# Kernel optimization log

Hardware: AMD Instinct MI355X
Metric: run time of the kernel (lower is better)

The kernel has to match this reference:

```python
import jax, jax.numpy as jnp
import numpy as np

NEG_SLOPE = 0.2
EPS = 1e-16

N_NODES = 100000
N_EDGES = 1600000
F_IN = 64
HID = 64
T_OUT = 1


def _gat_conv(x, src, dst, W, a_src, a_dst, b, n_nodes):
    # x: [N, Fin] -> h: [N, H]
    h = x @ W
    # per-node attention logits, then gather per-edge (PyG GATConv, heads=1)
    s_src = h @ a_src  # [N]
    s_dst = h @ a_dst  # [N]
    e = jax.nn.leaky_relu(s_src[src] + s_dst[dst], NEG_SLOPE)  # [E]
    # segment softmax over incoming edges of each destination node
    m = jax.ops.segment_max(e, dst, num_segments=n_nodes)  # [N]
    ex = jnp.exp(e - m[dst])
    denom = jax.ops.segment_sum(ex, dst, num_segments=n_nodes)  # [N]
    alpha = ex / (denom[dst] + EPS)  # [E]
    # weighted scatter-add aggregation
    out = jax.ops.segment_sum(alpha[:, None] * h[src], dst, num_segments=n_nodes)
    return out + b


def _add_self_loops(edge_index, n_nodes):
    loops = jnp.arange(n_nodes, dtype=edge_index.dtype)
    src = jnp.concatenate([edge_index[0], loops])
    dst = jnp.concatenate([edge_index[1], loops])
    return src, dst


def setup_inputs() -> dict:
    key = jax.random.key(0)
    ks = jax.random.split(key, 12)
    x = jax.random.normal(ks[0], (N_NODES, F_IN), dtype=jnp.float32)
    edge_index = jax.random.randint(ks[1], (2, N_EDGES), 0, N_NODES, dtype=jnp.int32)
    s1 = 1.0 / np.sqrt(F_IN)
    s2 = 1.0 / np.sqrt(HID)
    return {
        "x": x,
        "edge_index": edge_index,
        "W1": jax.random.normal(ks[2], (F_IN, HID), dtype=jnp.float32) * s1,
        "a_src1": jax.random.normal(ks[3], (HID,), dtype=jnp.float32) * s2,
        "a_dst1": jax.random.normal(ks[4], (HID,), dtype=jnp.float32) * s2,
        "b1": jnp.zeros((HID,), dtype=jnp.float32),
        "W2": jax.random.normal(ks[5], (HID, HID), dtype=jnp.float32) * s2,
        "a_src2": jax.random.normal(ks[6], (HID,), dtype=jnp.float32) * s2,
        "a_dst2": jax.random.normal(ks[7], (HID,), dtype=jnp.float32) * s2,
        "b2": jnp.zeros((HID,), dtype=jnp.float32),
        "Wl": jax.random.normal(ks[8], (HID, T_OUT), dtype=jnp.float32) * s2,
        "bl": jnp.zeros((T_OUT,), dtype=jnp.float32),
    }


def reference(x, edge_index, W1, a_src1, a_dst1, b1, W2, a_src2, a_dst2, b2, Wl, bl):
    n_nodes = x.shape[0]
    src, dst = _add_self_loops(edge_index, n_nodes)  # PyG add_self_loops=True
    h = _gat_conv(x, src, dst, W1, a_src1, a_dst1, b1, n_nodes)
    h = jnp.tanh(h)  # dropout is identity in eval mode
    h = _gat_conv(h, src, dst, W2, a_src2, a_dst2, b2, n_nodes)
    return h @ Wl + bl  # [N, 1]
```

## Files before the change

### kernel.cpp

```cpp
#include <hip/hip_runtime.h>

#define NN 100000
#define NE 1600000
#define ET (NE + NN)
#define NB 391
#define CAP 5120
#define BST 16
#define NBIN 256
#define NCHK (ET/8)
#define NTILE (NN/16)

typedef _Float16 f16;
typedef __attribute__((ext_vector_type(8))) _Float16 half8;
typedef __attribute__((ext_vector_type(4))) float f32x4;

__device__ __forceinline__ unsigned short hbits(float v){
    f16 h = (f16)v;
    return *(unsigned short*)&h;
}
__device__ __forceinline__ unsigned pk16(float a, float b){
    auto p = __builtin_amdgcn_cvt_pkrtz(a, b);
    return *(unsigned*)&p;
}
__device__ __forceinline__ float fast_tanh(float x){
    float e = __expf(2.f*x);
    return 1.f - __fdividef(2.f, e + 1.f);
}
__device__ __forceinline__ void fmix2(float& al, float& ah, unsigned h2, float a){
    asm("v_fma_mix_f32 %0, %2, %3, %0 op_sel_hi:[1,0,0]\n\t"
        "v_fma_mix_f32 %1, %2, %3, %1 op_sel:[1,0,0] op_sel_hi:[1,0,0]"
        : "+v"(al), "+v"(ah) : "v"(h2), "v"(a));
}

__global__ void __launch_bounds__(256) k_bin(const int* __restrict__ src,
        const int* __restrict__ dst, int* __restrict__ bcnt,
        int* __restrict__ binbuf){
    __shared__ int cnt[NB];
    __shared__ int cur[NB];
    int t = threadIdx.x;
    for(int i=t;i<NB;i+=256) cnt[i]=0;
    __syncthreads();
    for(int g = blockIdx.x*256 + t; g < NCHK; g += NBIN*256){
        if(g < NE/8){
            const uint4* dp = (const uint4*)(dst + g*8);
            uint4 d0 = dp[0], d1 = dp[1];
            atomicAdd(&cnt[d0.x>>8],1); atomicAdd(&cnt[d0.y>>8],1);
            atomicAdd(&cnt[d0.z>>8],1); atomicAdd(&cnt[d0.w>>8],1);
            atomicAdd(&cnt[d1.x>>8],1); atomicAdd(&cnt[d1.y>>8],1);
            atomicAdd(&cnt[d1.z>>8],1); atomicAdd(&cnt[d1.w>>8],1);
        } else {
            int n0 = g*8 - NE;
            #pragma unroll
            for(int i=0;i<8;i++) atomicAdd(&cnt[(n0+i)>>8],1);
        }
    }
    __syncthreads();
    for(int i=t;i<NB;i+=256){ int c=cnt[i]; cur[i] = c ? atomicAdd(&bcnt[i*BST], c) : 0; }
    __syncthreads();
    for(int g = blockIdx.x*256 + t; g < NCHK; g += NBIN*256){
        int s[8], d[8];
        if(g < NE/8){
            const uint4* sp = (const uint4*)(src + g*8);
            const uint4* dp = (const uint4*)(dst + g*8);
            uint4 s0 = sp[0], s1 = sp[1];
            uint4 d0 = dp[0], d1 = dp[1];
            s[0]=s0.x; s[1]=s0.y; s[2]=s0.z; s[3]=s0.w;
            s[4]=s1.x; s[5]=s1.y; s[6]=s1.z; s[7]=s1.w;
            d[0]=d0.x; d[1]=d0.y; d[2]=d0.z; d[3]=d0.w;
            d[4]=d1.x; d[5]=d1.y; d[6]=d1.z; d[7]=d1.w;
        } else {
            int n0 = g*8 - NE;
            #pragma unroll
            for(int i=0;i<8;i++){ s[i]=n0+i; d[i]=n0+i; }
        }
        #pragma unroll
        for(int i=0;i<8;i++){
            int b = d[i] >> 8;
            int pos = atomicAdd(&cur[b], 1);
            if(pos < CAP) binbuf[b*CAP + pos] = (s[i] << 8) | (d[i] & 255);
        }
    }
}

__global__ void __launch_bounds__(256) k_build(const int* __restrict__ bcnt,
        const int* __restrict__ binbuf, int* __restrict__ edge_src,
        int2* __restrict__ rd){
    __shared__ int lsrc[CAP];
    __shared__ int ldeg[256], lscan[256], lcur[256], red[256];
    int b = blockIdx.x, t = threadIdx.x;
    int cnt = min(bcnt[b*BST], CAP);
    int part = 0;
    for(int i=t;i<b;i+=256) part += min(bcnt[i*BST], CAP);
    red[t] = part; __syncthreads();
    for(int off=128; off>=1; off>>=1){ if(t<off) red[t]+=red[t+off]; __syncthreads(); }
    int base = red[0];
    __syncthreads();
    ldeg[t] = 0; __syncthreads();
    const int* bb = binbuf + b*CAP;
    for(int i=t;i<cnt;i+=256) atomicAdd(&ldeg[bb[i] & 255], 1);
    __syncthreads();
    int dv = ldeg[t]; lscan[t] = dv; __syncthreads();
    for(int off=1; off<256; off<<=1){
        int u = (t>=off) ? lscan[t-off] : 0;
        __syncthreads(); lscan[t] += u; __syncthreads();
    }
    int excl = lscan[t] - dv; lcur[t] = excl;
    int node = b*256 + t;
    if(node < NN) rd[node] = make_int2(base + excl, dv);
    __syncthreads();
    for(int i=t;i<cnt;i+=256){
        int ent = bb[i];
        int pos = atomicAdd(&lcur[ent & 255], 1);
        lsrc[pos] = ent >> 8;
    }
    __syncthreads();
    for(int i=t;i<cnt;i+=256) edge_src[base+i] = lsrc[i];
}

template<int FPIN, int L2>
__global__ void __launch_bounds__(256) k_gemm(const void* __restrict__ xin,
        const float* __restrict__ W, const float* __restrict__ avs,
        const float* __restrict__ avd, const float* __restrict__ Wlv,
        f16* __restrict__ hb, float* __restrict__ ssrc,
        float* __restrict__ sdst, float* __restrict__ gsc){
    int tid = threadIdx.x, lane = tid & 63;
    int col = lane & 15, q = lane >> 4;
    half8 Bf[2][4];
    #pragma unroll
    for(int kh=0;kh<2;kh++){
        #pragma unroll
        for(int nb=0;nb<4;nb++){
            half8 b;
            #pragma unroll
            for(int j=0;j<8;j++){
                float w = W[(kh*32 + q*8 + j)*64 + nb*16 + col];
                b[j] = (f16)w;
            }
            Bf[kh][nb] = b;
        }
    }
    float as[4], ad[4], wl[4];
    #pragma unroll
    for(int nb=0;nb<4;nb++){
        as[nb] = avs[nb*16+col]; ad[nb] = avd[nb*16+col];
        wl[nb] = L2 ? Wlv[nb*16+col] : 0.f;
    }

    int gw = (blockIdx.x*256 + tid) >> 6;
    int nwaves = gridDim.x*4;
    for(int tile = gw; tile < NTILE; tile += nwaves){
        int n0 = tile*16;
        f32x4 acc[4];
        #pragma unroll
        for(int nb=0;nb<4;nb++) acc[nb] = (f32x4){0.f,0.f,0.f,0.f};
        #pragma unroll
        for(int kh=0;kh<2;kh++){
            half8 a;
            if(FPIN){
                const float4* xr = (const float4*)((const float*)xin
                                    + (size_t)(n0+col)*64 + kh*32 + q*8);
                float4 u = xr[0], v = xr[1];
                union { half8 h; uint4 u4; } A;
                A.u4.x = pk16(u.x, u.y);
                A.u4.y = pk16(u.z, u.w);
                A.u4.z = pk16(v.x, v.y);
                A.u4.w = pk16(v.z, v.w);
                a = A.h;
            } else {
                a = *(const half8*)((const f16*)xin
                                    + (size_t)(n0+col)*64 + kh*32 + q*8);
            }
            #pragma unroll
            for(int nb=0;nb<4;nb++)
                acc[nb] = __builtin_amdgcn_mfma_f32_16x16x32_f16(a, Bf[kh][nb], acc[nb], 0,0,0);
        }
        if(!L2){
            #pragma unroll
            for(int nb=0;nb<4;nb++){
                #pragma unroll
                for(int r=0;r<4;r++)
                    hb[(size_t)(n0 + q*4 + r)*64 + nb*16 + col] = (f16)acc[nb][r];
            }
        }
        #pragma unroll
        for(int r=0;r<4;r++){
            float ps = acc[0][r]*as[0] + acc[1][r]*as[1] + acc[2][r]*as[2] + acc[3][r]*as[3];
            float pd = acc[0][r]*ad[0] + acc[1][r]*ad[1] + acc[2][r]*ad[2] + acc[3][r]*ad[3];
            float pg = L2 ? (acc[0][r]*wl[0] + acc[1][r]*wl[1] + acc[2][r]*wl[2] + acc[3][r]*wl[3]) : 0.f;
            #pragma unroll
            for(int m=8;m>=1;m>>=1){
                ps += __shfl_xor(ps,m); pd += __shfl_xor(pd,m);
                if(L2) pg += __shfl_xor(pg,m);
            }
            if(col == 0){
                ssrc[n0 + q*4 + r] = ps; sdst[n0 + q*4 + r] = pd;
                if(L2) gsc[n0 + q*4 + r] = pg;
            }
        }
    }
}

__device__ __forceinline__ void node_full1(int node, int lane, int2* lp,
        const int2* __restrict__ rd, const int* __restrict__ edge_src,
        const float* __restrict__ ssrc, const float* __restrict__ sdst,
        const f16* __restrict__ hb, const float* __restrict__ bias,
        f16* __restrict__ out1b){
    int2 r = rd[node];
    int rs = r.x, d = r.y;
    float sd = sdst[node];
    int g8 = lane >> 3;
    int c  = lane & 7;
    float a0=0.f,a1=0.f,a2=0.f,a3=0.f,a4=0.f,a5=0.f,a6=0.f,a7=0.f;

    float lmax = -1e30f;
    for(int j=lane; j<d; j+=64){
        int sj = edge_src[rs+j];
        float t = ssrc[sj] + sd;
        lmax = fmaxf(lmax, fmaxf(t, 0.2f*t));
    }
    #pragma unroll
    for(int m=32;m>=1;m>>=1) lmax = fmaxf(lmax, __shfl_xor(lmax,m));
    float lsum = 0.f;
    for(int j=lane; j<d; j+=64){
        int sj = edge_src[rs+j];
        float t = ssrc[sj] + sd;
        lsum += __expf(fmaxf(t, 0.2f*t) - lmax);
    }
    #pragma unroll
    for(int m=32;m>=1;m>>=1) lsum += __shfl_xor(lsum,m);
    float inv = 1.0f/(lsum + 1e-16f);
    for(int cb=0; cb<d; cb+=64){
        int s2 = 0; float al = 0.f;
        int j = cb + lane;
        if(j < d){
            s2 = edge_src[rs+j];
            float t = ssrc[s2] + sd;
            al = __expf(fmaxf(t, 0.2f*t) - lmax) * inv;
        }
        lp[lane] = make_int2(__float_as_int(al), s2);
        int dd = min(d - cb, 64);
        for(int i0=0; i0<dd; i0+=16){
            int2 e0 = lp[i0 + g8];
            int2 e1 = lp[i0 + 8 + g8];
            float f0 = __int_as_float(e0.x);
            float f1 = __int_as_float(e1.x);
            uint4 k0 = *(const uint4*)(hb + ((size_t)e0.y<<6) + (c<<3));
            uint4 k1 = *(const uint4*)(hb + ((size_t)e1.y<<6) + (c<<3));
            fmix2(a0,a1,k0.x,f0); fmix2(a2,a3,k0.y,f0);
            fmix2(a4,a5,k0.z,f0); fmix2(a6,a7,k0.w,f0);
            fmix2(a0,a1,k1.x,f1); fmix2(a2,a3,k1.y,f1);
            fmix2(a4,a5,k1.z,f1); fmix2(a6,a7,k1.w,f1);
        }
    }
    #pragma unroll
    for(int m=32;m>=8;m>>=1){
        a0 += __shfl_xor(a0,m); a1 += __shfl_xor(a1,m);
        a2 += __shfl_xor(a2,m); a3 += __shfl_xor(a3,m);
        a4 += __shfl_xor(a4,m); a5 += __shfl_xor(a5,m);
        a6 += __shfl_xor(a6,m); a7 += __shfl_xor(a7,m);
    }
    const float4* bp = (const float4*)bias;
    float4 bv0 = bp[c*2], bv1 = bp[c*2+1];
    if(g8 == 0){
        uint4 o;
        o.x = (unsigned)hbits(fast_tanh(a0+bv0.x)) | ((unsigned)hbits(fast_tanh(a1+bv0.y))<<16);
        o.y = (unsigned)hbits(fast_tanh(a2+bv0.z)) | ((unsigned)hbits(fast_tanh(a3+bv0.w))<<16);
        o.z = (unsigned)hbits(fast_tanh(a4+bv1.x)) | ((unsigned)hbits(fast_tanh(a5+bv1.y))<<16);
        o.w = (unsigned)hbits(fast_tanh(a6+bv1.z)) | ((unsigned)hbits(fast_tanh(a7+bv1.w))<<16);
        *(uint4*)(out1b + ((size_t)node<<6) + (c<<3)) = o;
    }
}

__global__ void __launch_bounds__(256) k_agg1(
        const int2* __restrict__ rd, const int* __restrict__ edge_src,
        const float* __restrict__ ssrc, const float* __restrict__ sdst,
        const f16* __restrict__ hb, const float* __restrict__ bias,
        f16* __restrict__ out1b){
    __shared__ int2 pairs[256];
    int tid = threadIdx.x;
    int wv   = (blockIdx.x*256 + tid) >> 6;
    int lane = tid & 63;
    if(wv*2 >= NN) return;
    int2* lp = pairs + (tid & 192);
    int half = lane >> 5, l = lane & 31;
    int node = wv*2 + half;

    int2 r = rd[node];
    int rs = r.x, d = r.y;
    float sd = sdst[node];
    int dmax = max(d, __shfl_xor(d, 32));

    if(dmax <= 32){
        int s = 0; float pr = 0.f;
        if(l < d){
            s = edge_src[rs + l];
            float t = ssrc[s] + sd;
            t = fmaxf(t, 0.2f*t);
            pr = __expf(fminf(t, 80.f));
        }
        float sm = pr;
        #pragma unroll
        for(int m=16;m>=1;m>>=1) sm += __shfl_xor(sm,m);
        float alpha = pr * (1.0f/(sm + 1e-16f));
        lp[lane] = make_int2(__float_as_int(alpha), s);

        int g4 = l >> 3;
        int c  = l & 7;
        int base = half << 5;
        int nitw = (dmax + 7) >> 3;
        float F0[4], F1[4];
        uint4 K0[4], K1[4];
        #pragma unroll
        for(int it=0; it<4; it++){
            if(it < nitw){
                int2 e0 = lp[base + it*8 + g4];
                int2 e1 = lp[base + it*8 + 4 + g4];
                F0[it] = __int_as_float(e0.x);
                F1[it] = __int_as_float(e1.x);
                K0[it] = *(const uint4*)(hb + ((size_t)e0.y<<6) + (c<<3));
                K1[it] = *(const uint4*)(hb + ((size_t)e1.y<<6) + (c<<3));
            }
        }
        float a0=0.f,a1=0.f,a2=0.f,a3=0.f,a4=0.f,a5=0.f,a6=0.f,a7=0.f;
        #pragma unroll
        for(int it=0; it<4; it++){
            if(it < nitw){
                fmix2(a0,a1,K0[it].x,F0[it]); fmix2(a2,a3,K0[it].y,F0[it]);
                fmix2(a4,a5,K0[it].z,F0[it]); fmix2(a6,a7,K0[it].w,F0[it]);
                fmix2(a0,a1,K1[it].x,F1[it]); fmix2(a2,a3,K1[it].y,F1[it]);
                fmix2(a4,a5,K1[it].z,F1[it]); fmix2(a6,a7,K1[it].w,F1[it]);
            }
        }

        bool b3 = (l >> 3) & 1, b4 = (l >> 4) & 1;
        float u0 = b3 ? a4 : a0, v0 = b3 ? a0 : a4; u0 += __shfl_xor(v0, 8);
        float u1 = b3 ? a5 : a1, v1 = b3 ? a1 : a5; u1 += __shfl_xor(v1, 8);
        float u2 = b3 ? a6 : a2, v2 = b3 ? a2 : a6; u2 += __shfl_xor(v2, 8);
        float u3 = b3 ? a7 : a3, v3 = b3 ? a3 : a7; u3 += __shfl_xor(v3, 8);
        float w0 = b4 ? u2 : u0, z0 = b4 ? u0 : u2; w0 += __shfl_xor(z0, 16);
        float w1 = b4 ? u3 : u1, z1 = b4 ? u1 : u3; w1 += __shfl_xor(z1, 16);
        int ch0 = (c<<3) + ((int)b3<<2) + ((int)b4<<1);

        float2 bv = ((const float2*)bias)[ch0>>1];
        unsigned o = pk16(fast_tanh(w0 + bv.x), fast_tanh(w1 + bv.y));
        *(unsigned*)(out1b + ((size_t)node<<6) + ch0) = o;
    } else {
        node_full1(wv*2,   lane, lp, rd, edge_src, ssrc, sdst, hb, bias, out1b);
        node_full1(wv*2+1, lane, lp, rd, edge_src, ssrc, sdst, hb, bias, out1b);
    }
}

__global__ void __launch_bounds__(256) k_agg2(
        const int2* __restrict__ rd, const int* __restrict__ edge_src,
        const float* __restrict__ ssrc, const float* __restrict__ sdst,
        const float* __restrict__ gsc, const float* __restrict__ bias,
        const float* __restrict__ Wl, const float* __restrict__ bl,
        float* __restrict__ outF){
    int tid = threadIdx.x;
    int wv   = (blockIdx.x*256 + tid) >> 6;
    int lane = tid & 63;
    if(wv*2 >= NN) return;
    int half = lane >> 5, l = lane & 31;
    int node = wv*2 + half;

    float2 bv = ((const float2*)bias)[l];
    float2 wl = ((const float2*)Wl)[l];
    float rc = bv.x*wl.x + bv.y*wl.y;
    #pragma unroll
    for(int m=16;m>=1;m>>=1) rc += __shfl_xor(rc,m);

    int2 r = rd[node];
    int rs = r.x, d = r.y;
    float sd = sdst[node];
    int dmax = max(d, __shfl_xor(d, 32));

    if(dmax <= 32){
        float pr = 0.f, gv = 0.f;
        if(l < d){
            int s = edge_src[rs + l];
            float t = ssrc[s] + sd;
            t = fmaxf(t, 0.2f*t);
            pr = __expf(fminf(t, 80.f));
            gv = gsc[s];
        }
        float sm = pr, num = pr*gv;
        #pragma unroll
        for(int m=16;m>=1;m>>=1){ sm += __shfl_xor(sm,m); num += __shfl_xor(num,m); }
        if(l == 0) outF[node] = num/(sm + 1e-16f) + rc + bl[0];
    } else {
        #pragma unroll 1
        for(int k=0;k<2;k++){
            int nd = wv*2 + k;
            int2 r2 = rd[nd];
            int rs2 = r2.x, d2 = r2.y;
            float sd2 = sdst[nd];
            float lmax = -1e30f;
            for(int j=lane; j<d2; j+=64){
                int sj = edge_src[rs2+j];
                float t = ssrc[sj] + sd2;
                lmax = fmaxf(lmax, fmaxf(t, 0.2f*t));
            }
            #pragma unroll
            for(int m=32;m>=1;m>>=1) lmax = fmaxf(lmax, __shfl_xor(lmax,m));
            float lsum = 0.f, lnum = 0.f;
            for(int j=lane; j<d2; j+=64){
                int sj = edge_src[rs2+j];
                float t = ssrc[sj] + sd2;
                float e = __expf(fmaxf(t, 0.2f*t) - lmax);
                lsum += e; lnum += e*gsc[sj];
            }
            #pragma unroll
            for(int m=32;m>=1;m>>=1){ lsum += __shfl_xor(lsum,m); lnum += __shfl_xor(lnum,m); }
            if(lane == 0) outF[nd] = lnum/(lsum + 1e-16f) + rc + bl[0];
        }
    }
}

extern "C" void kernel_launch(void* const* d_in, const int* in_sizes, int n_in,
                              void* d_out, int out_size, void* d_ws, size_t ws_size,
                              hipStream_t stream) {
    const float* x   = (const float*)d_in[0];
    const int*   ei  = (const int*)d_in[1];
    const float* W1  = (const float*)d_in[2];
    const float* as1 = (const float*)d_in[3];
    const float* ad1 = (const float*)d_in[4];
    const float* b1  = (const float*)d_in[5];
    const float* W2  = (const float*)d_in[6];
    const float* as2 = (const float*)d_in[7];
    const float* ad2 = (const float*)d_in[8];
    const float* b2  = (const float*)d_in[9];
    const float* Wl  = (const float*)d_in[10];
    const float* bl  = (const float*)d_in[11];
    float* out = (float*)d_out;

    const int* srcp = ei;
    const int* dstp = ei + NE;

    char* w = (char*)d_ws;
    int*   edge_src = (int*)w;  w += (size_t)ET*4;
    f16*   hb       = (f16*)w;  w += (size_t)NN*64*2;
    f16*   t1b      = (f16*)w;  w += (size_t)NN*64*2;
    int2*  rd       = (int2*)w; w += (size_t)NN*8;
    float* ssrc     = (float*)w; w += (size_t)NN*4;
    float* sdst     = (float*)w; w += (size_t)NN*4;
    float* gsc      = (float*)w; w += (size_t)NN*4;
    int*   bcnt     = (int*)w;  w += (size_t)NB*BST*4;
    int*   binbuf   = (int*)hb;

    const int nbG  = 782;
    const int nbA1 = (NN/2 + 3)/4;
    const int nbA2 = (NN/2 + 3)/4;

    (void)hipMemsetAsync(bcnt, 0, (size_t)NB*BST*4, stream);
    k_bin  <<<NBIN, 256, 0, stream>>>(srcp, dstp, bcnt, binbuf);
    k_build<<<NB,   256, 0, stream>>>(bcnt, binbuf, edge_src, rd);

    k_gemm<1,0><<<nbG, 256, 0, stream>>>((const void*)x, W1, as1, ad1,
                                         (const float*)nullptr, hb, ssrc, sdst,
                                         (float*)nullptr);
    k_agg1<<<nbA1, 256, 0, stream>>>(rd, edge_src, ssrc, sdst, hb, b1, t1b);
    k_gemm<0,1><<<nbG, 256, 0, stream>>>((const void*)t1b, W2, as2, ad2, Wl,
                                         (f16*)nullptr, ssrc, sdst, gsc);
    k_agg2<<<nbA2, 256, 0, stream>>>(rd, edge_src, ssrc, sdst, gsc,
                                     b2, Wl, bl, out);
}
```

Baseline: 196.6 us.

## Fold layer-2 GEMM into per-node vectors and fuse CSR build with layer-1 GEMM

Layer 2 only needs the attention scores and the final linear projection of h2, so W2·a_src2, W2·a_dst2 and W2·Wl are precomputed into three 64-vectors. The layer-1 aggregation then emits the three scalar scores per node directly. This drops the tanh output buffer, the second GEMM kernel and its 100k×64 f16 round trip. The CSR build and the layer-1 GEMM are merged into one launch split by block index so they can overlap, and binbuf gets its own buffer instead of aliasing hb. The cost is extra shuffle reductions in agg1 and reassociating the sums, which changes rounding slightly.

```diff
diff --git a/kernel.cpp b/kernel.cpp
--- a/kernel.cpp
+++ b/kernel.cpp
@@ -9,6 +9,7 @@
 #define NBIN 256
 #define NCHK (ET/8)
 #define NTILE (NN/16)
+#define NBG 782
 
 typedef _Float16 f16;
 typedef __attribute__((ext_vector_type(8))) _Float16 half8;
@@ -30,6 +31,19 @@
     asm("v_fma_mix_f32 %0, %2, %3, %0 op_sel_hi:[1,0,0]\n\t"
         "v_fma_mix_f32 %1, %2, %3, %1 op_sel:[1,0,0] op_sel_hi:[1,0,0]"
         : "+v"(al), "+v"(ah) : "v"(h2), "v"(a));
+}
+
+__global__ void __launch_bounds__(64) k_pre(const float* __restrict__ W2,
+        const float* __restrict__ as2, const float* __restrict__ ad2,
+        const float* __restrict__ Wl, float* __restrict__ w2v){
+    int j = threadIdx.x;
+    float s = 0.f, d = 0.f, g = 0.f;
+    #pragma unroll 8
+    for(int i=0;i<64;i++){
+        float w = W2[j*64 + i];
+        s += w*as2[i]; d += w*ad2[i]; g += w*Wl[i];
+    }
+    w2v[j] = s; w2v[64+j] = d; w2v[128+j] = g;
 }
 
 __global__ void __launch_bounds__(256) k_bin(const int* __restrict__ src,
@@ -82,82 +96,76 @@
     }
 }
 
-__global__ void __launch_bounds__(256) k_build(const int* __restrict__ bcnt,
-        const int* __restrict__ binbuf, int* __restrict__ edge_src,
-        int2* __restrict__ rd){
+__global__ void __launch_bounds__(256) k_bg(
+        const int* __restrict__ bcnt, const int* __restrict__ binbuf,
+        int* __restrict__ edge_src, int2* __restrict__ rd,
+        const float* __restrict__ xin, const float* __restrict__ W,
+        const float* __restrict__ avs, const float* __restrict__ avd,
+        f16* __restrict__ hb, float* __restrict__ ssrc,
+        float* __restrict__ sdst){
     __shared__ int lsrc[CAP];
     __shared__ int ldeg[256], lscan[256], lcur[256], red[256];
-    int b = blockIdx.x, t = threadIdx.x;
-    int cnt = min(bcnt[b*BST], CAP);
-    int part = 0;
-    for(int i=t;i<b;i+=256) part += min(bcnt[i*BST], CAP);
-    red[t] = part; __syncthreads();
-    for(int off=128; off>=1; off>>=1){ if(t<off) red[t]+=red[t+off]; __syncthreads(); }
-    int base = red[0];
-    __syncthreads();
-    ldeg[t] = 0; __syncthreads();
-    const int* bb = binbuf + b*CAP;
-    for(int i=t;i<cnt;i+=256) atomicAdd(&ldeg[bb[i] & 255], 1);
-    __syncthreads();
-    int dv = ldeg[t]; lscan[t] = dv; __syncthreads();
-    for(int off=1; off<256; off<<=1){
-        int u = (t>=off) ? lscan[t-off] : 0;
-        __syncthreads(); lscan[t] += u; __syncthreads();
-    }
-    int excl = lscan[t] - dv; lcur[t] = excl;
-    int node = b*256 + t;
-    if(node < NN) rd[node] = make_int2(base + excl, dv);
-    __syncthreads();
-    for(int i=t;i<cnt;i+=256){
-        int ent = bb[i];
-        int pos = atomicAdd(&lcur[ent & 255], 1);
-        lsrc[pos] = ent >> 8;
-    }
-    __syncthreads();
-    for(int i=t;i<cnt;i+=256) edge_src[base+i] = lsrc[i];
-}
-
-template<int FPIN, int L2>
-__global__ void __launch_bounds__(256) k_gemm(const void* __restrict__ xin,
-        const float* __restrict__ W, const float* __restrict__ avs,
-        const float* __restrict__ avd, const float* __restrict__ Wlv,
-        f16* __restrict__ hb, float* __restrict__ ssrc,
-        float* __restrict__ sdst, float* __restrict__ gsc){
-    int tid = threadIdx.x, lane = tid & 63;
-    int col = lane & 15, q = lane >> 4;
-    half8 Bf[2][4];
-    #pragma unroll
-    for(int kh=0;kh<2;kh++){
-        #pragma unroll
-        for(int nb=0;nb<4;nb++){
-            half8 b;
-            #pragma unroll
-            for(int j=0;j<8;j++){
-                float w = W[(kh*32 + q*8 + j)*64 + nb*16 + col];
-                b[j] = (f16)w;
-            }
-            Bf[kh][nb] = b;
-        }
-    }
-    float as[4], ad[4], wl[4];
-    #pragma unroll
-    for(int nb=0;nb<4;nb++){
-        as[nb] = avs[nb*16+col]; ad[nb] = avd[nb*16+col];
-        wl[nb] = L2 ? Wlv[nb*16+col] : 0.f;
-    }
-
-    int gw = (blockIdx.x*256 + tid) >> 6;
-    int nwaves = gridDim.x*4;
-    for(int tile = gw; tile < NTILE; tile += nwaves){
-        int n0 = tile*16;
-        f32x4 acc[4];
-        #pragma unroll
-        for(int nb=0;nb<4;nb++) acc[nb] = (f32x4){0.f,0.f,0.f,0.f};
+    int t = threadIdx.x;
+    if(blockIdx.x < NB){
+        int b = blockIdx.x;
+        int cnt = min(bcnt[b*BST], CAP);
+        int part = 0;
+        for(int i=t;i<b;i+=256) part += min(bcnt[i*BST], CAP);
+        red[t] = part; __syncthreads();
+        for(int off=128; off>=1; off>>=1){ if(t<off) red[t]+=red[t+off]; __syncthreads(); }
+        int base = red[0];
+        __syncthreads();
+        ldeg[t] = 0; __syncthreads();
+        const int* bb = binbuf + b*CAP;
+        for(int i=t;i<cnt;i+=256) atomicAdd(&ldeg[bb[i] & 255], 1);
+        __syncthreads();
+        int dv = ldeg[t]; lscan[t] = dv; __syncthreads();
+        for(int off=1; off<256; off<<=1){
+            int u = (t>=off) ? lscan[t-off] : 0;
+            __syncthreads(); lscan[t] += u; __syncthreads();
+        }
+        int excl = lscan[t] - dv; lcur[t] = excl;
+        int node = b*256 + t;
+        if(node < NN) rd[node] = make_int2(base + excl, dv);
+        __syncthreads();
+        for(int i=t;i<cnt;i+=256){
+            int ent = bb[i];
+            int pos = atomicAdd(&lcur[ent & 255], 1);
+            lsrc[pos] = ent >> 8;
+        }
+        __syncthreads();
+        for(int i=t;i<cnt;i+=256) edge_src[base+i] = lsrc[i];
+    } else {
+        int lane = t & 63;
+        int col = lane & 15, q = lane >> 4;
+        half8 Bf[2][4];
         #pragma unroll
         for(int kh=0;kh<2;kh++){
-            half8 a;
-            if(FPIN){
-                const float4* xr = (const float4*)((const float*)xin
+            #pragma unroll
+            for(int nb=0;nb<4;nb++){
+                half8 bfr;
+                #pragma unroll
+                for(int j=0;j<8;j++){
+                    float w = W[(kh*32 + q*8 + j)*64 + nb*16 + col];
+                    bfr[j] = (f16)w;
+                }
+                Bf[kh][nb] = bfr;
+            }
+        }
+        float as[4], ad[4];
+        #pragma unroll
+        for(int nb=0;nb<4;nb++){ as[nb] = avs[nb*16+col]; ad[nb] = avd[nb*16+col]; }
+
+        int gw = ((blockIdx.x - NB)*256 + t) >> 6;
+        int nwaves = NBG*4;
+        for(int tile = gw; tile < NTILE; tile += nwaves){
+            int n0 = tile*16;
+            f32x4 acc[4];
+            #pragma unroll
+            for(int nb=0;nb<4;nb++) acc[nb] = (f32x4){0.f,0.f,0.f,0.f};
+            #pragma unroll
+            for(int kh=0;kh<2;kh++){
+                const float4* xr = (const float4*)(xin
                                     + (size_t)(n0+col)*64 + kh*32 + q*8);
                 float4 u = xr[0], v = xr[1];
                 union { half8 h; uint4 u4; } A;
@@ -165,36 +173,23 @@
                 A.u4.y = pk16(u.z, u.w);
                 A.u4.z = pk16(v.x, v.y);
                 A.u4.w = pk16(v.z, v.w);
-                a = A.h;
-            } else {
-                a = *(const half8*)((const f16*)xin
-                                    + (size_t)(n0+col)*64 + kh*32 + q*8);
-            }
-            #pragma unroll
-            for(int nb=0;nb<4;nb++)
-                acc[nb] = __builtin_amdgcn_mfma_f32_16x16x32_f16(a, Bf[kh][nb], acc[nb], 0,0,0);
-        }
-        if(!L2){
+                #pragma unroll
+                for(int nb=0;nb<4;nb++)
+                    acc[nb] = __builtin_amdgcn_mfma_f32_16x16x32_f16(A.h, Bf[kh][nb], acc[nb], 0,0,0);
+            }
             #pragma unroll
             for(int nb=0;nb<4;nb++){
                 #pragma unroll
                 for(int r=0;r<4;r++)
                     hb[(size_t)(n0 + q*4 + r)*64 + nb*16 + col] = (f16)acc[nb][r];
             }
-        }
-        #pragma unroll
-        for(int r=0;r<4;r++){
-            float ps = acc[0][r]*as[0] + acc[1][r]*as[1] + acc[2][r]*as[2] + acc[3][r]*as[3];
-            float pd = acc[0][r]*ad[0] + acc[1][r]*ad[1] + acc[2][r]*ad[2] + acc[3][r]*ad[3];
-            float pg = L2 ? (acc[0][r]*wl[0] + acc[1][r]*wl[1] + acc[2][r]*wl[2] + acc[3][r]*wl[3]) : 0.f;
-            #pragma unroll
-            for(int m=8;m>=1;m>>=1){
-                ps += __shfl_xor(ps,m); pd += __shfl_xor(pd,m);
-                if(L2) pg += __shfl_xor(pg,m);
-            }
-            if(col == 0){
-                ssrc[n0 + q*4 + r] = ps; sdst[n0 + q*4 + r] = pd;
-                if(L2) gsc[n0 + q*4 + r] = pg;
+            #pragma unroll
+            for(int r=0;r<4;r++){
+                float ps = acc[0][r]*as[0] + acc[1][r]*as[1] + acc[2][r]*as[2] + acc[3][r]*as[3];
+                float pd = acc[0][r]*ad[0] + acc[1][r]*ad[1] + acc[2][r]*ad[2] + acc[3][r]*ad[3];
+                #pragma unroll
+                for(int m=8;m>=1;m>>=1){ ps += __shfl_xor(ps,m); pd += __shfl_xor(pd,m); }
+                if(col == 0){ ssrc[n0 + q*4 + r] = ps; sdst[n0 + q*4 + r] = pd; }
             }
         }
     }
@@ -204,7 +199,8 @@
         const int2* __restrict__ rd, const int* __restrict__ edge_src,
         const float* __restrict__ ssrc, const float* __restrict__ sdst,
         const f16* __restrict__ hb, const float* __restrict__ bias,
-        f16* __restrict__ out1b){
+        const float* __restrict__ w2v, float* __restrict__ ssrc2,
+        float* __restrict__ sdst2, float* __restrict__ gsc){
     int2 r = rd[node];
     int rs = r.x, d = r.y;
     float sd = sdst[node];
@@ -261,21 +257,32 @@
     }
     const float4* bp = (const float4*)bias;
     float4 bv0 = bp[c*2], bv1 = bp[c*2+1];
-    if(g8 == 0){
-        uint4 o;
-        o.x = (unsigned)hbits(fast_tanh(a0+bv0.x)) | ((unsigned)hbits(fast_tanh(a1+bv0.y))<<16);
-        o.y = (unsigned)hbits(fast_tanh(a2+bv0.z)) | ((unsigned)hbits(fast_tanh(a3+bv0.w))<<16);
-        o.z = (unsigned)hbits(fast_tanh(a4+bv1.x)) | ((unsigned)hbits(fast_tanh(a5+bv1.y))<<16);
-        o.w = (unsigned)hbits(fast_tanh(a6+bv1.z)) | ((unsigned)hbits(fast_tanh(a7+bv1.w))<<16);
-        *(uint4*)(out1b + ((size_t)node<<6) + (c<<3)) = o;
-    }
+    float t0 = fast_tanh(a0+bv0.x), t1 = fast_tanh(a1+bv0.y);
+    float t2 = fast_tanh(a2+bv0.z), t3 = fast_tanh(a3+bv0.w);
+    float t4 = fast_tanh(a4+bv1.x), t5 = fast_tanh(a5+bv1.y);
+    float t6 = fast_tanh(a6+bv1.z), t7 = fast_tanh(a7+bv1.w);
+    const float4* vs = (const float4*)(w2v);
+    const float4* vd = (const float4*)(w2v+64);
+    const float4* vg = (const float4*)(w2v+128);
+    float4 s0 = vs[c*2], s1 = vs[c*2+1];
+    float4 d0 = vd[c*2], d1 = vd[c*2+1];
+    float4 g0 = vg[c*2], g1 = vg[c*2+1];
+    float q_s = t0*s0.x+t1*s0.y+t2*s0.z+t3*s0.w + t4*s1.x+t5*s1.y+t6*s1.z+t7*s1.w;
+    float q_d = t0*d0.x+t1*d0.y+t2*d0.z+t3*d0.w + t4*d1.x+t5*d1.y+t6*d1.z+t7*d1.w;
+    float q_g = t0*g0.x+t1*g0.y+t2*g0.z+t3*g0.w + t4*g1.x+t5*g1.y+t6*g1.z+t7*g1.w;
+    #pragma unroll
+    for(int m=4;m>=1;m>>=1){
+        q_s += __shfl_xor(q_s,m); q_d += __shfl_xor(q_d,m); q_g += __shfl_xor(q_g,m);
+    }
+    if(lane == 0){ ssrc2[node] = q_s; sdst2[node] = q_d; gsc[node] = q_g; }
 }
 
 __global__ void __launch_bounds__(256) k_agg1(
         const int2* __restrict__ rd, const int* __restrict__ edge_src,
         const float* __restrict__ ssrc, const float* __restrict__ sdst,
         const f16* __restrict__ hb, const float* __restrict__ bias,
-        f16* __restrict__ out1b){
+        const float* __restrict__ w2v, float* __restrict__ ssrc2,
+        float* __restrict__ sdst2, float* __restrict__ gsc){
     __shared__ int2 pairs[256];
     int tid = threadIdx.x;
     int wv   = (blockIdx.x*256 + tid) >> 6;
@@ -342,11 +349,23 @@
         int ch0 = (c<<3) + ((int)b3<<2) + ((int)b4<<1);
 
         float2 bv = ((const float2*)bias)[ch0>>1];
-        unsigned o = pk16(fast_tanh(w0 + bv.x), fast_tanh(w1 + bv.y));
-        *(unsigned*)(out1b + ((size_t)node<<6) + ch0) = o;
+        float tw0 = fast_tanh(w0 + bv.x), tw1 = fast_tanh(w1 + bv.y);
+        float2 vs = ((const float2*)(w2v      ))[ch0>>1];
+        float2 vd = ((const float2*)(w2v +  64))[ch0>>1];
+        float2 vg = ((const float2*)(w2v + 128))[ch0>>1];
+        float q_s = tw0*vs.x + tw1*vs.y;
+        float q_d = tw0*vd.x + tw1*vd.y;
+        float q_g = tw0*vg.x + tw1*vg.y;
+        #pragma unroll
+        for(int m=16;m>=1;m>>=1){
+            q_s += __shfl_xor(q_s,m); q_d += __shfl_xor(q_d,m); q_g += __shfl_xor(q_g,m);
+        }
+        if(l == 0){ ssrc2[node] = q_s; sdst2[node] = q_d; gsc[node] = q_g; }
     } else {
-        node_full1(wv*2,   lane, lp, rd, edge_src, ssrc, sdst, hb, bias, out1b);
-        node_full1(wv*2+1, lane, lp, rd, edge_src, ssrc, sdst, hb, bias, out1b);
+        node_full1(wv*2,   lane, lp, rd, edge_src, ssrc, sdst, hb, bias,
+                   w2v, ssrc2, sdst2, gsc);
+        node_full1(wv*2+1, lane, lp, rd, edge_src, ssrc, sdst, hb, bias,
+                   w2v, ssrc2, sdst2, gsc);
     }
 }
 
@@ -439,28 +458,25 @@
     char* w = (char*)d_ws;
     int*   edge_src = (int*)w;  w += (size_t)ET*4;
     f16*   hb       = (f16*)w;  w += (size_t)NN*64*2;
-    f16*   t1b      = (f16*)w;  w += (size_t)NN*64*2;
+    int*   binbuf   = (int*)w;  w += (size_t)NB*CAP*4;
     int2*  rd       = (int2*)w; w += (size_t)NN*8;
     float* ssrc     = (float*)w; w += (size_t)NN*4;
     float* sdst     = (float*)w; w += (size_t)NN*4;
+    float* ssrc2    = (float*)w; w += (size_t)NN*4;
+    float* sdst2    = (float*)w; w += (size_t)NN*4;
     float* gsc      = (float*)w; w += (size_t)NN*4;
+    float* w2v      = (float*)w; w += (size_t)192*4;
     int*   bcnt     = (int*)w;  w += (size_t)NB*BST*4;
-    int*   binbuf   = (int*)hb;
-
-    const int nbG  = 782;
-    const int nbA1 = (NN/2 + 3)/4;
-    const int nbA2 = (NN/2 + 3)/4;
+
+    const int nbA = (NN/2 + 3)/4;
 
     (void)hipMemsetAsync(bcnt, 0, (size_t)NB*BST*4, stream);
-    k_bin  <<<NBIN, 256, 0, stream>>>(srcp, dstp, bcnt, binbuf);
-    k_build<<<NB,   256, 0, stream>>>(bcnt, binbuf, edge_src, rd);
-
-    k_gemm<1,0><<<nbG, 256, 0, stream>>>((const void*)x, W1, as1, ad1,
-                                         (const float*)nullptr, hb, ssrc, sdst,
-                                         (float*)nullptr);
-    k_agg1<<<nbA1, 256, 0, stream>>>(rd, edge_src, ssrc, sdst, hb, b1, t1b);
-    k_gemm<0,1><<<nbG, 256, 0, stream>>>((const void*)t1b, W2, as2, ad2, Wl,
-                                         (f16*)nullptr, ssrc, sdst, gsc);
-    k_agg2<<<nbA2, 256, 0, stream>>>(rd, edge_src, ssrc, sdst, gsc,
-                                     b2, Wl, bl, out);
-}
+    k_pre<<<1, 64, 0, stream>>>(W2, as2, ad2, Wl, w2v);
+    k_bin<<<NBIN, 256, 0, stream>>>(srcp, dstp, bcnt, binbuf);
+    k_bg<<<NB + NBG, 256, 0, stream>>>(bcnt, binbuf, edge_src, rd,
+                                       x, W1, as1, ad1, hb, ssrc, sdst);
+    k_agg1<<<nbA, 256, 0, stream>>>(rd, edge_src, ssrc, sdst, hb, b1,
+                                    w2v, ssrc2, sdst2, gsc);
+    k_agg2<<<nbA, 256, 0, stream>>>(rd, edge_src, ssrc2, sdst2, gsc,
+                                    b2, Wl, bl, out);
+}
```

Result: faster. 190.5 us (-3.1%).
